# Performance work log

Measured on AMD Instinct MI355X. Metric: run time of the kernel, lower is better.

Reference implementation:

```python
import jax, jax.numpy as jnp
import numpy as np

B, S, D, H = 2, 2048, 1024, 16
DK = D // H  # 64


def setup_inputs() -> dict:
    key = jax.random.key(0)
    ks = jax.random.split(key, 9)
    s = 0.02
    return {
        "embeddings": jax.random.normal(ks[0], (B, S, D), jnp.float32),
        "Wq": jax.random.normal(ks[1], (H, D, DK), jnp.float32) * s,
        "bq": jax.random.normal(ks[2], (H, DK), jnp.float32) * s,
        "Wk": jax.random.normal(ks[3], (H, D, DK), jnp.float32) * s,
        "bk": jax.random.normal(ks[4], (H, DK), jnp.float32) * s,
        "Wv": jax.random.normal(ks[5], (H, D, DK), jnp.float32) * s,
        "bv": jax.random.normal(ks[6], (H, DK), jnp.float32) * s,
        "Wo": jax.random.normal(ks[7], (D, D), jnp.float32) * s,
        "bo": jax.random.normal(ks[8], (D,), jnp.float32) * s,
    }


def reference(embeddings, Wq, bq, Wk, bk, Wv, bv, Wo, bo):
    b, s, d = embeddings.shape
    dk = Wq.shape[-1]
    # batched per-head projections: [b,s,d] x [h,d,k] -> [b,h,s,k]
    q = jnp.einsum('bsd,hdk->bhsk', embeddings, Wq) + bq[None, :, None, :]
    k = jnp.einsum('bsd,hdk->bhsk', embeddings, Wk) + bk[None, :, None, :]
    v = jnp.einsum('bsd,hdk->bhsk', embeddings, Wv) + bv[None, :, None, :]
    scores = jnp.einsum('bhqk,bhsk->bhqs', q, k) / jnp.sqrt(jnp.float32(dk))
    causal_mask = jnp.triu(jnp.ones((s, s), dtype=bool), k=1)  # True above diagonal
    scores = jnp.where(causal_mask, jnp.float32(-1e9), scores)
    weights = jax.nn.softmax(scores, axis=-1)
    ctx = jnp.einsum('bhqs,bhsk->bhqk', weights, v)
    concat = ctx.transpose(0, 2, 1, 3).reshape(b, s, d)  # head-major concat, matches torch.cat
    return concat @ Wo + bo
```

## Files before the change

### kernel.cpp

```cpp
#include <hip/hip_runtime.h>
#include <hip/hip_bf16.h>

typedef unsigned short u16;
typedef unsigned int u32;
typedef __bf16 bf16x8 __attribute__((ext_vector_type(8)));
typedef float f32x4 __attribute__((ext_vector_type(4)));

#define AS1 __attribute__((address_space(1)))
#define AS3 __attribute__((address_space(3)))

#define NB 2
#define NS 2048
#define ND 1024
#define NH 16
#define NK 64

__device__ __forceinline__ u16 f2bf(float f) {
  u32 u = __builtin_bit_cast(u32, f);
  return (u16)((u + 0x7FFFu + ((u >> 16) & 1u)) >> 16);
}

__device__ __forceinline__ void stage_tile(u16* lds, const u16* __restrict__ src, int rs,
                                           int wid, int lane) {
#pragma unroll
  for (int i = 0; i < 2; ++i) {
    int c = wid * 128 + i * 64 + lane;
    int row = c >> 3;
    int kc = (c & 7) ^ (row & 7);
    __builtin_amdgcn_global_load_lds((const AS1 u32*)(src + row * rs + kc * 8),
                                     (AS3 u32*)(lds + (wid * 128 + i * 64) * 8), 16, 0, 0);
  }
}

__device__ __forceinline__ bf16x8 read_frag(const u16* lds, int row, int ks, int lane) {
  int slot = ((lane >> 4) + ks * 4) ^ (row & 7);
  return *(const bf16x8*)(lds + row * 64 + slot * 8);
}

__global__ __launch_bounds__(256) void convert_kernel(const float* __restrict__ src,
                                                      u16* __restrict__ dst, int n) {
  int i = (blockIdx.x * 256 + threadIdx.x) * 4;
  if (i >= n) return;
  float4 v = *(const float4*)(src + i);
  u32 w0 = (u32)f2bf(v.x) | ((u32)f2bf(v.y) << 16);
  u32 w1 = (u32)f2bf(v.z) | ((u32)f2bf(v.w) << 16);
  uint2 w; w.x = w0; w.y = w1;
  *(uint2*)(dst + i) = w;
}

__global__ __launch_bounds__(256) void transpose_conv(const float* __restrict__ src,
                                                      u16* __restrict__ dst, int R, int C) {
  __shared__ float tile[32][33];
  size_t base = (size_t)blockIdx.z * R * C;
  src += base;
  dst += base;
  int c0 = blockIdx.x * 32, r0 = blockIdx.y * 32;
  int tx = threadIdx.x, ty = threadIdx.y;
#pragma unroll
  for (int i = 0; i < 4; ++i)
    tile[ty + 8 * i][tx] = src[(size_t)(r0 + ty + 8 * i) * C + c0 + tx];
  __syncthreads();
#pragma unroll
  for (int i = 0; i < 4; ++i)
    dst[(size_t)(c0 + ty + 8 * i) * R + r0 + tx] = f2bf(tile[tx][ty + 8 * i]);
}

__global__ __launch_bounds__(256) void qkv_kernel(
    const u16* __restrict__ emb, const u16* __restrict__ Wqt, const u16* __restrict__ Wkt,
    const u16* __restrict__ Wvt, const float* __restrict__ bq, const float* __restrict__ bk,
    const float* __restrict__ bv, u16* __restrict__ Q, u16* __restrict__ K,
    u16* __restrict__ Vt) {
  __shared__ alignas(16) u16 lds_a[64 * 64];
  __shared__ alignas(16) u16 lds_b[64 * 64];
  int tid = threadIdx.x, lane = tid & 63, wid = tid >> 6;
  int mt = blockIdx.x, h = blockIdx.y, which = blockIdx.z;
  const u16* Wt = (which == 0 ? Wqt : which == 1 ? Wkt : Wvt) + h * (ND * NK);
  const float* bias = (which == 0 ? bq : which == 1 ? bk : bv) + h * NK;
  int m0 = mt * 64;
  int col = lane & 15;
  f32x4 zero4 = {0.f, 0.f, 0.f, 0.f};
  f32x4 acc[4] = {zero4, zero4, zero4, zero4};
  for (int k0 = 0; k0 < ND; k0 += 64) {
    stage_tile(lds_a, emb + m0 * ND + k0, ND, wid, lane);
    stage_tile(lds_b, Wt + k0, ND, wid, lane);
    __syncthreads();
#pragma unroll
    for (int ks = 0; ks < 2; ++ks) {
      bf16x8 a = read_frag(lds_a, wid * 16 + col, ks, lane);
#pragma unroll
      for (int f = 0; f < 4; ++f) {
        bf16x8 b = read_frag(lds_b, f * 16 + col, ks, lane);
        acc[f] = __builtin_amdgcn_mfma_f32_16x16x32_bf16(a, b, acc[f], 0, 0, 0);
      }
    }
    __syncthreads();
  }
  int rbase = m0 + wid * 16 + (lane >> 4) * 4;
#pragma unroll
  for (int f = 0; f < 4; ++f) {
    int n = f * 16 + col;
    float bn = bias[n];
#pragma unroll
    for (int r = 0; r < 4; ++r) {
      int m = rbase + r;
      int b = m >> 11, s = m & (NS - 1);
      float v = acc[f][r] + bn;
      if (which == 0) {
        Q[((b * NH + h) * NS + s) * NK + n] = f2bf(v * 0.125f);
      } else if (which == 1) {
        K[((b * NH + h) * NS + s) * NK + n] = f2bf(v);
      } else {
        Vt[((b * NH + h) * NK + n) * NS + s] = f2bf(v);
      }
    }
  }
}

__global__ __launch_bounds__(256) void attn_kernel(const u16* __restrict__ Q,
                                                   const u16* __restrict__ K,
                                                   const u16* __restrict__ Vt,
                                                   u16* __restrict__ ctx) {
  __shared__ alignas(16) u16 lds_k[2][64 * 64];
  __shared__ alignas(16) u16 lds_v[2][64 * 64];
  __shared__ alignas(16) u16 p_lds[4][16 * 72];
  int tid = threadIdx.x, lane = tid & 63, wid = tid >> 6;
  int bh = blockIdx.x;
  int qt = (int)gridDim.y - 1 - (int)blockIdx.y;
  const u16* Qb = Q + bh * (NS * NK);
  const u16* Kb = K + bh * (NS * NK);
  const u16* Vb = Vt + bh * (NK * NS);
  int q0 = qt * 64;
  int col = lane & 15;
  int qrow_a = q0 + wid * 16 + col;
  bf16x8 qf0 = *(const bf16x8*)(Qb + qrow_a * NK + (lane >> 4) * 8);
  bf16x8 qf1 = *(const bf16x8*)(Qb + qrow_a * NK + 32 + (lane >> 4) * 8);
  f32x4 zero4 = {0.f, 0.f, 0.f, 0.f};
  f32x4 acc[4] = {zero4, zero4, zero4, zero4};
  float m[4], l[4];
#pragma unroll
  for (int r = 0; r < 4; ++r) { m[r] = -1e30f; l[r] = 0.f; }
  int qrow_c = q0 + wid * 16 + (lane >> 4) * 4;
  u16* pw = p_lds[wid];
  int nt = qt + 1;

  stage_tile(lds_k[0], Kb, NK, wid, lane);
  stage_tile(lds_v[0], Vb, NS, wid, lane);
  __syncthreads();

  for (int t = 0; t < nt; ++t) {
    int cur = t & 1;
    if (t + 1 < nt) {
      stage_tile(lds_k[cur ^ 1], Kb + (t + 1) * 64 * NK, NK, wid, lane);
      stage_tile(lds_v[cur ^ 1], Vb + (t + 1) * 64, NS, wid, lane);
    }
    const u16* lk = lds_k[cur];
    const u16* lv = lds_v[cur];
    f32x4 sc[4];
#pragma unroll
    for (int f = 0; f < 4; ++f) {
      bf16x8 b0 = read_frag(lk, f * 16 + col, 0, lane);
      sc[f] = __builtin_amdgcn_mfma_f32_16x16x32_bf16(qf0, b0, zero4, 0, 0, 0);
      bf16x8 b1 = read_frag(lk, f * 16 + col, 1, lane);
      sc[f] = __builtin_amdgcn_mfma_f32_16x16x32_bf16(qf1, b1, sc[f], 0, 0, 0);
    }
    if (t == qt) {
#pragma unroll
      for (int f = 0; f < 4; ++f) {
        int kg = t * 64 + f * 16 + col;
#pragma unroll
        for (int r = 0; r < 4; ++r)
          if (kg > qrow_c + r) sc[f][r] = -1e30f;
      }
    }
    float mx[4];
#pragma unroll
    for (int r = 0; r < 4; ++r)
      mx[r] = fmaxf(fmaxf(sc[0][r], sc[1][r]), fmaxf(sc[2][r], sc[3][r]));
#pragma unroll
    for (int off = 1; off < 16; off <<= 1)
#pragma unroll
      for (int r = 0; r < 4; ++r) mx[r] = fmaxf(mx[r], __shfl_xor(mx[r], off));
    float alpha[4];
#pragma unroll
    for (int r = 0; r < 4; ++r) {
      float mn = fmaxf(m[r], mx[r]);
      alpha[r] = exp2f((m[r] - mn) * 1.44269504f);
      m[r] = mn;
    }
    float rs[4] = {0.f, 0.f, 0.f, 0.f};
#pragma unroll
    for (int f = 0; f < 4; ++f)
#pragma unroll
      for (int r = 0; r < 4; ++r) {
        float p = exp2f((sc[f][r] - m[r]) * 1.44269504f);
        sc[f][r] = p;
        rs[r] += p;
      }
#pragma unroll
    for (int off = 1; off < 16; off <<= 1)
#pragma unroll
      for (int r = 0; r < 4; ++r) rs[r] += __shfl_xor(rs[r], off);
#pragma unroll
    for (int r = 0; r < 4; ++r) l[r] = l[r] * alpha[r] + rs[r];
#pragma unroll
    for (int f = 0; f < 4; ++f)
#pragma unroll
      for (int r = 0; r < 4; ++r) acc[f][r] *= alpha[r];
#pragma unroll
    for (int f = 0; f < 4; ++f)
#pragma unroll
      for (int r = 0; r < 4; ++r)
        pw[((lane >> 4) * 4 + r) * 72 + f * 16 + col] = f2bf(sc[f][r]);
#pragma unroll
    for (int ks = 0; ks < 2; ++ks) {
      bf16x8 pa = *(const bf16x8*)(pw + col * 72 + ks * 32 + (lane >> 4) * 8);
#pragma unroll
      for (int f = 0; f < 4; ++f) {
        bf16x8 vb = read_frag(lv, f * 16 + col, ks, lane);
        acc[f] = __builtin_amdgcn_mfma_f32_16x16x32_bf16(pa, vb, acc[f], 0, 0, 0);
      }
    }
    __syncthreads();
  }
  int b = bh >> 4, h = bh & 15;
#pragma unroll
  for (int r = 0; r < 4; ++r) {
    float inv = 1.0f / l[r];
    int s = qrow_c + r;
#pragma unroll
    for (int f = 0; f < 4; ++f)
      ctx[(b * NS + s) * ND + h * NK + f * 16 + col] = f2bf(acc[f][r] * inv);
  }
}

__global__ __launch_bounds__(256) void outproj_kernel(const u16* __restrict__ ctx,
                                                      const u16* __restrict__ Wot,
                                                      const float* __restrict__ bo,
                                                      float* __restrict__ out) {
  __shared__ alignas(16) u16 lds_a[64 * 64];
  __shared__ alignas(16) u16 lds_b[64 * 64];
  int tid = threadIdx.x, lane = tid & 63, wid = tid >> 6;
  int m0 = blockIdx.x * 64, n0 = blockIdx.y * 64;
  int col = lane & 15;
  f32x4 zero4 = {0.f, 0.f, 0.f, 0.f};
  f32x4 acc[4] = {zero4, zero4, zero4, zero4};
  for (int k0 = 0; k0 < ND; k0 += 64) {
    stage_tile(lds_a, ctx + m0 * ND + k0, ND, wid, lane);
    stage_tile(lds_b, Wot + n0 * ND + k0, ND, wid, lane);
    __syncthreads();
#pragma unroll
    for (int ks = 0; ks < 2; ++ks) {
      bf16x8 a = read_frag(lds_a, wid * 16 + col, ks, lane);
#pragma unroll
      for (int f = 0; f < 4; ++f) {
        bf16x8 b = read_frag(lds_b, f * 16 + col, ks, lane);
        acc[f] = __builtin_amdgcn_mfma_f32_16x16x32_bf16(a, b, acc[f], 0, 0, 0);
      }
    }
    __syncthreads();
  }
  int rbase = m0 + wid * 16 + (lane >> 4) * 4;
#pragma unroll
  for (int f = 0; f < 4; ++f) {
    int n = n0 + f * 16 + col;
    float bn = bo[n];
#pragma unroll
    for (int r = 0; r < 4; ++r) out[(rbase + r) * ND + n] = acc[f][r] + bn;
  }
}

extern "C" void kernel_launch(void* const* d_in, const int* in_sizes, int n_in,
                              void* d_out, int out_size, void* d_ws, size_t ws_size,
                              hipStream_t stream) {
  (void)in_sizes; (void)n_in; (void)out_size;
  const float* emb = (const float*)d_in[0];
  const float* Wq = (const float*)d_in[1];
  const float* bq = (const float*)d_in[2];
  const float* Wk = (const float*)d_in[3];
  const float* bk = (const float*)d_in[4];
  const float* Wv = (const float*)d_in[5];
  const float* bv = (const float*)d_in[6];
  const float* Wo = (const float*)d_in[7];
  const float* bo = (const float*)d_in[8];
  float* out = (float*)d_out;

  const size_t EMB_N = (size_t)NB * NS * ND;
  const size_t W_N = (size_t)NH * ND * NK;
  const size_t QKV_N = (size_t)NB * NH * NS * NK;
  if (ws_size < (EMB_N + 4 * W_N + 3 * QKV_N) * sizeof(u16)) return;
  u16* ws = (u16*)d_ws;
  u16* emb_bf = ws;
  u16* Wqt = emb_bf + EMB_N;
  u16* Wkt = Wqt + W_N;
  u16* Wvt = Wkt + W_N;
  u16* Wot = Wvt + W_N;
  u16* Qb = Wot + W_N;
  u16* Kb = Qb + QKV_N;
  u16* Vtb = Kb + QKV_N;
  u16* ctxb = emb_bf;

  convert_kernel<<<dim3((int)(EMB_N / 4 / 256)), dim3(256), 0, stream>>>(emb, emb_bf,
                                                                         (int)EMB_N);
  dim3 tb(32, 8);
  transpose_conv<<<dim3(2, 32, 16), tb, 0, stream>>>(Wq, Wqt, ND, NK);
  transpose_conv<<<dim3(2, 32, 16), tb, 0, stream>>>(Wk, Wkt, ND, NK);
  transpose_conv<<<dim3(2, 32, 16), tb, 0, stream>>>(Wv, Wvt, ND, NK);
  transpose_conv<<<dim3(32, 32, 1), tb, 0, stream>>>(Wo, Wot, ND, ND);
  qkv_kernel<<<dim3(64, 16, 3), dim3(256), 0, stream>>>(emb_bf, Wqt, Wkt, Wvt, bq, bk, bv,
                                                        Qb, Kb, Vtb);
  attn_kernel<<<dim3(32, 32), dim3(256), 0, stream>>>(Qb, Kb, Vtb, ctxb);
  outproj_kernel<<<dim3(64, 16), dim3(256), 0, stream>>>(ctxb, Wot, bo, out);
}
```

Measured before the change: 146.3 us.

## Pair causal query tiles per block and add lazy softmax rescaling

```diff
diff --git a/kernel.cpp b/kernel.cpp
--- a/kernel.cpp
+++ b/kernel.cpp
@@ -18,6 +18,12 @@
 __device__ __forceinline__ u16 f2bf(float f) {
   u32 u = __builtin_bit_cast(u32, f);
   return (u16)((u + 0x7FFFu + ((u >> 16) & 1u)) >> 16);
+}
+
+__device__ __forceinline__ u32 cvt_pk_bf16(float lo, float hi) {
+  u32 u;
+  asm("v_cvt_pk_bf16_f32 %0, %1, %2" : "=v"(u) : "v"(lo), "v"(hi));
+  return u;
 }
 
 __device__ __forceinline__ void stage_tile(u16* lds, const u16* __restrict__ src, int rs,
@@ -42,8 +48,8 @@
   int i = (blockIdx.x * 256 + threadIdx.x) * 4;
   if (i >= n) return;
   float4 v = *(const float4*)(src + i);
-  u32 w0 = (u32)f2bf(v.x) | ((u32)f2bf(v.y) << 16);
-  u32 w1 = (u32)f2bf(v.z) | ((u32)f2bf(v.w) << 16);
+  u32 w0 = cvt_pk_bf16(v.x, v.y);
+  u32 w1 = cvt_pk_bf16(v.z, v.w);
   uint2 w; w.x = w0; w.y = w1;
   *(uint2*)(dst + i) = w;
 }
@@ -106,7 +112,7 @@
       int b = m >> 11, s = m & (NS - 1);
       float v = acc[f][r] + bn;
       if (which == 0) {
-        Q[((b * NH + h) * NS + s) * NK + n] = f2bf(v * 0.125f);
+        Q[((b * NH + h) * NS + s) * NK + n] = f2bf(v * 0.18033688f);
       } else if (which == 1) {
         K[((b * NH + h) * NS + s) * NK + n] = f2bf(v);
       } else {
@@ -125,111 +131,120 @@
   __shared__ alignas(16) u16 p_lds[4][16 * 72];
   int tid = threadIdx.x, lane = tid & 63, wid = tid >> 6;
   int bh = blockIdx.x;
-  int qt = (int)gridDim.y - 1 - (int)blockIdx.y;
+  int pr = blockIdx.y;
   const u16* Qb = Q + bh * (NS * NK);
   const u16* Kb = K + bh * (NS * NK);
   const u16* Vb = Vt + bh * (NK * NS);
-  int q0 = qt * 64;
   int col = lane & 15;
-  int qrow_a = q0 + wid * 16 + col;
-  bf16x8 qf0 = *(const bf16x8*)(Qb + qrow_a * NK + (lane >> 4) * 8);
-  bf16x8 qf1 = *(const bf16x8*)(Qb + qrow_a * NK + 32 + (lane >> 4) * 8);
+  int b = bh >> 4, h = bh & 15;
   f32x4 zero4 = {0.f, 0.f, 0.f, 0.f};
-  f32x4 acc[4] = {zero4, zero4, zero4, zero4};
-  float m[4], l[4];
-#pragma unroll
-  for (int r = 0; r < 4; ++r) { m[r] = -1e30f; l[r] = 0.f; }
-  int qrow_c = q0 + wid * 16 + (lane >> 4) * 4;
   u16* pw = p_lds[wid];
-  int nt = qt + 1;
-
-  stage_tile(lds_k[0], Kb, NK, wid, lane);
-  stage_tile(lds_v[0], Vb, NS, wid, lane);
-  __syncthreads();
-
-  for (int t = 0; t < nt; ++t) {
-    int cur = t & 1;
-    if (t + 1 < nt) {
-      stage_tile(lds_k[cur ^ 1], Kb + (t + 1) * 64 * NK, NK, wid, lane);
-      stage_tile(lds_v[cur ^ 1], Vb + (t + 1) * 64, NS, wid, lane);
-    }
-    const u16* lk = lds_k[cur];
-    const u16* lv = lds_v[cur];
-    f32x4 sc[4];
-#pragma unroll
-    for (int f = 0; f < 4; ++f) {
-      bf16x8 b0 = read_frag(lk, f * 16 + col, 0, lane);
-      sc[f] = __builtin_amdgcn_mfma_f32_16x16x32_bf16(qf0, b0, zero4, 0, 0, 0);
-      bf16x8 b1 = read_frag(lk, f * 16 + col, 1, lane);
-      sc[f] = __builtin_amdgcn_mfma_f32_16x16x32_bf16(qf1, b1, sc[f], 0, 0, 0);
-    }
-    if (t == qt) {
+
+#pragma unroll 1
+  for (int half = 0; half < 2; ++half) {
+    int qt = half ? pr : (31 - pr);
+    int q0 = qt * 64;
+    int qrow_a = q0 + wid * 16 + col;
+    bf16x8 qf0 = *(const bf16x8*)(Qb + qrow_a * NK + (lane >> 4) * 8);
+    bf16x8 qf1 = *(const bf16x8*)(Qb + qrow_a * NK + 32 + (lane >> 4) * 8);
+    f32x4 acc[4] = {zero4, zero4, zero4, zero4};
+    float m[4], lp[4];
+#pragma unroll
+    for (int r = 0; r < 4; ++r) { m[r] = -1e30f; lp[r] = 0.f; }
+    int qrow_c = q0 + wid * 16 + (lane >> 4) * 4;
+    int nt = qt + 1;
+
+    stage_tile(lds_k[0], Kb, NK, wid, lane);
+    stage_tile(lds_v[0], Vb, NS, wid, lane);
+    __syncthreads();
+
+    for (int t = 0; t < nt; ++t) {
+      int cur = t & 1;
+      if (t + 1 < nt) {
+        stage_tile(lds_k[cur ^ 1], Kb + (t + 1) * 64 * NK, NK, wid, lane);
+        stage_tile(lds_v[cur ^ 1], Vb + (t + 1) * 64, NS, wid, lane);
+      }
+      const u16* lk = lds_k[cur];
+      const u16* lv = lds_v[cur];
+      f32x4 sc[4];
 #pragma unroll
       for (int f = 0; f < 4; ++f) {
-        int kg = t * 64 + f * 16 + col;
-#pragma unroll
-        for (int r = 0; r < 4; ++r)
-          if (kg > qrow_c + r) sc[f][r] = -1e30f;
-      }
-    }
-    float mx[4];
-#pragma unroll
-    for (int r = 0; r < 4; ++r)
-      mx[r] = fmaxf(fmaxf(sc[0][r], sc[1][r]), fmaxf(sc[2][r], sc[3][r]));
+        bf16x8 b0 = read_frag(lk, f * 16 + col, 0, lane);
+        sc[f] = __builtin_amdgcn_mfma_f32_16x16x32_bf16(qf0, b0, zero4, 0, 0, 0);
+        bf16x8 b1 = read_frag(lk, f * 16 + col, 1, lane);
+        sc[f] = __builtin_amdgcn_mfma_f32_16x16x32_bf16(qf1, b1, sc[f], 0, 0, 0);
+      }
+      if (t == qt) {
+#pragma unroll
+        for (int f = 0; f < 4; ++f) {
+          int kg = t * 64 + f * 16 + col;
+#pragma unroll
+          for (int r = 0; r < 4; ++r)
+            if (kg > qrow_c + r) sc[f][r] = -1e30f;
+        }
+      }
+      float mx[4];
+#pragma unroll
+      for (int r = 0; r < 4; ++r)
+        mx[r] = fmaxf(fmaxf(sc[0][r], sc[1][r]), fmaxf(sc[2][r], sc[3][r]));
+#pragma unroll
+      for (int off = 1; off < 16; off <<= 1)
+#pragma unroll
+        for (int r = 0; r < 4; ++r) mx[r] = fmaxf(mx[r], __shfl_xor(mx[r], off));
+      bool ok = true;
+#pragma unroll
+      for (int r = 0; r < 4; ++r) ok = ok && (mx[r] <= m[r] + 8.0f);
+      if (!__all(ok)) {
+#pragma unroll
+        for (int r = 0; r < 4; ++r) {
+          float mn = fmaxf(m[r], mx[r]);
+          float al = exp2f(m[r] - mn);
+          m[r] = mn;
+          lp[r] *= al;
+#pragma unroll
+          for (int f = 0; f < 4; ++f) acc[f][r] *= al;
+        }
+      }
+#pragma unroll
+      for (int f = 0; f < 4; ++f)
+#pragma unroll
+        for (int r = 0; r < 4; ++r) {
+          float p = exp2f(sc[f][r] - m[r]);
+          sc[f][r] = p;
+          lp[r] += p;
+        }
+#pragma unroll
+      for (int f = 0; f < 4; ++f)
+#pragma unroll
+        for (int rp = 0; rp < 4; rp += 2) {
+          u32 u = cvt_pk_bf16(sc[f][rp], sc[f][rp + 1]);
+          int row = (lane >> 4) * 4 + rp;
+          pw[row * 72 + f * 16 + col] = (u16)u;
+          pw[(row + 1) * 72 + f * 16 + col] = (u16)(u >> 16);
+        }
+#pragma unroll
+      for (int ks = 0; ks < 2; ++ks) {
+        bf16x8 pa = *(const bf16x8*)(pw + col * 72 + ks * 32 + (lane >> 4) * 8);
+#pragma unroll
+        for (int f = 0; f < 4; ++f) {
+          bf16x8 vb = read_frag(lv, f * 16 + col, ks, lane);
+          acc[f] = __builtin_amdgcn_mfma_f32_16x16x32_bf16(pa, vb, acc[f], 0, 0, 0);
+        }
+      }
+      __syncthreads();
+    }
 #pragma unroll
     for (int off = 1; off < 16; off <<= 1)
 #pragma unroll
-      for (int r = 0; r < 4; ++r) mx[r] = fmaxf(mx[r], __shfl_xor(mx[r], off));
-    float alpha[4];
+      for (int r = 0; r < 4; ++r) lp[r] += __shfl_xor(lp[r], off);
 #pragma unroll
     for (int r = 0; r < 4; ++r) {
-      float mn = fmaxf(m[r], mx[r]);
-      alpha[r] = exp2f((m[r] - mn) * 1.44269504f);
-      m[r] = mn;
-    }
-    float rs[4] = {0.f, 0.f, 0.f, 0.f};
-#pragma unroll
-    for (int f = 0; f < 4; ++f)
-#pragma unroll
-      for (int r = 0; r < 4; ++r) {
-        float p = exp2f((sc[f][r] - m[r]) * 1.44269504f);
-        sc[f][r] = p;
-        rs[r] += p;
-      }
-#pragma unroll
-    for (int off = 1; off < 16; off <<= 1)
-#pragma unroll
-      for (int r = 0; r < 4; ++r) rs[r] += __shfl_xor(rs[r], off);
-#pragma unroll
-    for (int r = 0; r < 4; ++r) l[r] = l[r] * alpha[r] + rs[r];
-#pragma unroll
-    for (int f = 0; f < 4; ++f)
-#pragma unroll
-      for (int r = 0; r < 4; ++r) acc[f][r] *= alpha[r];
-#pragma unroll
-    for (int f = 0; f < 4; ++f)
-#pragma unroll
-      for (int r = 0; r < 4; ++r)
-        pw[((lane >> 4) * 4 + r) * 72 + f * 16 + col] = f2bf(sc[f][r]);
-#pragma unroll
-    for (int ks = 0; ks < 2; ++ks) {
-      bf16x8 pa = *(const bf16x8*)(pw + col * 72 + ks * 32 + (lane >> 4) * 8);
-#pragma unroll
-      for (int f = 0; f < 4; ++f) {
-        bf16x8 vb = read_frag(lv, f * 16 + col, ks, lane);
-        acc[f] = __builtin_amdgcn_mfma_f32_16x16x32_bf16(pa, vb, acc[f], 0, 0, 0);
-      }
-    }
-    __syncthreads();
-  }
-  int b = bh >> 4, h = bh & 15;
-#pragma unroll
-  for (int r = 0; r < 4; ++r) {
-    float inv = 1.0f / l[r];
-    int s = qrow_c + r;
-#pragma unroll
-    for (int f = 0; f < 4; ++f)
-      ctx[(b * NS + s) * ND + h * NK + f * 16 + col] = f2bf(acc[f][r] * inv);
+      float inv = 1.0f / lp[r];
+      int s = qrow_c + r;
+#pragma unroll
+      for (int f = 0; f < 4; ++f)
+        ctx[(b * NS + s) * ND + h * NK + f * 16 + col] = f2bf(acc[f][r] * inv);
+    }
   }
 }
 
@@ -308,6 +323,6 @@
   transpose_conv<<<dim3(32, 32, 1), tb, 0, stream>>>(Wo, Wot, ND, ND);
   qkv_kernel<<<dim3(64, 16, 3), dim3(256), 0, stream>>>(emb_bf, Wqt, Wkt, Wvt, bq, bk, bv,
                                                         Qb, Kb, Vtb);
-  attn_kernel<<<dim3(32, 32), dim3(256), 0, stream>>>(Qb, Kb, Vtb, ctxb);
+  attn_kernel<<<dim3(32, 16), dim3(256), 0, stream>>>(Qb, Kb, Vtb, ctxb);
   outproj_kernel<<<dim3(64, 16), dim3(256), 0, stream>>>(ctxb, Wot, bo, out);
 }
```

Result: faster. 139.6 us (-4.6%).
